# Kernel tuning notes

Measured on AMD Instinct MI355X. Metric: run time of the kernel, lower is better.

The kernel has to match this reference:

```python
import jax, jax.numpy as jnp
import numpy as np

PAD_MAG = 1e12
EPS = 1e-7  # matches prev_step.add_(1e-07) in the torch code


def setup_inputs() -> dict:
    key = jax.random.key(0)
    k1, k2, k3, k4 = jax.random.split(key, 4)
    B, txt_T, mel_T, n_mel = 16, 320, 2000, 80
    mu_logvar = jax.random.normal(k1, (B, txt_T, 2 * n_mel), dtype=jnp.float32)
    melspec = jax.random.normal(k2, (B, n_mel, mel_T), dtype=jnp.float32)
    text_lengths = jax.random.randint(k3, (B,), txt_T // 2, txt_T + 1).astype(jnp.int32)
    mel_lengths = jax.random.randint(k4, (B,), mel_T // 2, mel_T + 1).astype(jnp.int32)
    return {"mu_logvar": mu_logvar, "melspec": melspec,
            "text_lengths": text_lengths, "mel_lengths": mel_lengths}


def _log_prob_matrix(mu_logvar, melspec):
    # exponential[b,j,t] = -0.5 * mean_c( (x[b,t,c]-mu[b,j,c])^2 / exp(logvar) + logvar )
    # avoiding the [B,txt_T,mel_T,n_mel] broadcast the torch code materializes.
    n_mel = melspec.shape[1]
    mu = mu_logvar[:, :, :n_mel]          # [B, txt_T, n_mel]
    logvar = mu_logvar[:, :, n_mel:]      # [B, txt_T, n_mel]
    x = jnp.swapaxes(melspec, 1, 2)       # [B, mel_T, n_mel]
    inv_var = jnp.exp(-logvar)
    xx = jnp.einsum('btc,bjc->bjt', x * x, inv_var)
    xm = jnp.einsum('btc,bjc->bjt', x, mu * inv_var)
    mm = jnp.sum(mu * mu * inv_var + logvar, axis=2)  # [B, txt_T]
    return (-0.5 / n_mel) * (xx - 2.0 * xm + mm[:, :, None])  # [B, txt_T, mel_T]


def _forward_dp(log_prob, text_lengths, mel_lengths):
    # monotonic alignment forward algorithm (logsumexp DP over mel frames)
    B, txt_T, mel_T = log_prob.shape
    # carry = log_alpha column of size txt_T+1 (row 0 is the -inf pad row)
    init = jnp.full((B, txt_T + 1), -PAD_MAG, log_prob.dtype)
    init = init.at[:, 1].set(log_prob[:, 0, 0])

    def step(a, lp):  # a: [B, txt_T+1], lp: [B, txt_T]
        prev = jnp.stack([a[:, 1:], a[:, :-1]], axis=-1) + EPS
        tail = jax.nn.logsumexp(prev, axis=-1) + lp      # [B, txt_T]
        a_new = jnp.concatenate(
            [jnp.full((B, 1), -PAD_MAG, a.dtype), tail], axis=1)
        return a_new, tail

    lps = jnp.moveaxis(log_prob[:, :, 1:], 2, 0)         # [mel_T-1, B, txt_T]
    _, tails = jax.lax.scan(step, init, lps)             # [mel_T-1, B, txt_T]
    log_alpha = jnp.concatenate([init[None, :, 1:], tails], axis=0)  # [mel_T, B, txt_T]
    log_alpha = jnp.moveaxis(log_alpha, 0, 2)            # [B, txt_T, mel_T]

    bidx = jnp.arange(B)
    alpha_last = log_alpha[bidx, text_lengths - 1, mel_lengths - 1]
    alpha_last = alpha_last / mel_lengths.astype(log_alpha.dtype)
    return -jnp.mean(alpha_last)


def reference(mu_logvar, melspec, text_lengths, mel_lengths):
    log_prob = _log_prob_matrix(mu_logvar, melspec)
    mdn_loss = _forward_dp(log_prob, text_lengths, mel_lengths)
    return (mdn_loss, log_prob)
```

## Files before the change

### kernel.cpp

```cpp
#include <hip/hip_runtime.h>

#define BATCH 16
#define TXT   320
#define NMELC 80
#define MELT  2000
#define PADM  1.0e12f
#define L2E   1.4426950408889634f
#define LN2   0.6931471805599453f
#define EPSL2 1.4426950e-7f

typedef __attribute__((ext_vector_type(8))) short bf16x8;
typedef __attribute__((ext_vector_type(4))) float f32x4;

__device__ __forceinline__ short f2bf(float x) {
    unsigned u = __float_as_uint(x);
    unsigned r = (u + 0x7FFFu + ((u >> 16) & 1u)) >> 16;
    return (short)r;
}

__global__ __launch_bounds__(256) void lp_kernel(
    const float* __restrict__ mlv,
    const float* __restrict__ ms,
    float* __restrict__ out_lp)
{
    __shared__ short Ash[20][64][8];
    __shared__ short Bsh[20][128][8];
    __shared__ float bias_p[256];
    __shared__ float bias_s[64];

    const int b   = blockIdx.z;
    const int j0  = blockIdx.y * 64;
    const int t0  = blockIdx.x * 128;
    const int tid = threadIdx.x;
    const float s = -0.00625f;

    const float* mlv_b = mlv + (size_t)b * TXT * 160;
    const float* ms_b  = ms  + (size_t)b * NMELC * MELT;

    {
        const int jj = tid >> 2;
        const int q  = tid & 3;
        const float* p = mlv_b + (size_t)(j0 + jj) * 160 + q * 20;
        float part = 0.f;
        #pragma unroll
        for (int c = 0; c < 20; ++c) {
            float mu = p[c];
            float lv = p[c + 80];
            float iv = __expf(-lv);
            part += mu * mu * iv + lv;
        }
        bias_p[tid] = part;
    }
    __syncthreads();
    if (tid < 64) {
        float v = bias_p[tid * 4] + bias_p[tid * 4 + 1] +
                  bias_p[tid * 4 + 2] + bias_p[tid * 4 + 3];
        bias_s[tid] = s * v;
    }

    #pragma unroll
    for (int pass = 0; pass < 20; ++pass) {
        int idx = pass * 256 + tid;
        int j = idx / 80;
        int c = idx - j * 80;
        float mu = mlv_b[(size_t)(j0 + j) * 160 + c];
        float lv = mlv_b[(size_t)(j0 + j) * 160 + 80 + c];
        float iv = __expf(-lv);
        Ash[c >> 3][j][c & 7]        = f2bf(s * iv);
        Ash[10 + (c >> 3)][j][c & 7] = f2bf(-2.f * s * mu * iv);
    }
    #pragma unroll
    for (int pass = 0; pass < 10; ++pass) {
        int c   = pass * 8 + (tid >> 5);
        int t4i = tid & 31;
        int t   = t0 + t4i * 4;
        float xv[4];
        if (t + 3 < MELT) {
            float4 v = *(const float4*)&ms_b[(size_t)c * MELT + t];
            xv[0] = v.x; xv[1] = v.y; xv[2] = v.z; xv[3] = v.w;
        } else {
            #pragma unroll
            for (int i = 0; i < 4; ++i)
                xv[i] = (t + i < MELT) ? ms_b[(size_t)c * MELT + t + i] : 0.f;
        }
        #pragma unroll
        for (int i = 0; i < 4; ++i) {
            Bsh[c >> 3][t4i * 4 + i][c & 7]        = f2bf(xv[i] * xv[i]);
            Bsh[10 + (c >> 3)][t4i * 4 + i][c & 7] = f2bf(xv[i]);
        }
    }
    __syncthreads();

    const int wv = tid >> 6;
    const int l  = tid & 63;
    const int lr = l & 15;
    const int lg = l >> 4;

    f32x4 acc[8];
    #pragma unroll
    for (int f = 0; f < 8; ++f) acc[f] = (f32x4){0.f, 0.f, 0.f, 0.f};

    #pragma unroll
    for (int ks = 0; ks < 5; ++ks) {
        const int kb = ks * 4 + lg;
        bf16x8 a = *(const bf16x8*)&Ash[kb][wv * 16 + lr][0];
        #pragma unroll
        for (int f = 0; f < 8; ++f) {
            bf16x8 bb = *(const bf16x8*)&Bsh[kb][f * 16 + lr][0];
            acc[f] = __builtin_amdgcn_mfma_f32_16x16x32_bf16(a, bb, acc[f],
                                                             0, 0, 0);
        }
    }

    float bs[4];
    #pragma unroll
    for (int r = 0; r < 4; ++r) bs[r] = bias_s[wv * 16 + lg * 4 + r];
    #pragma unroll
    for (int f = 0; f < 8; ++f) {
        int t = t0 + f * 16 + lr;
        if (t < MELT) {
            #pragma unroll
            for (int r = 0; r < 4; ++r) {
                int j = j0 + wv * 16 + lg * 4 + r;
                out_lp[((size_t)b * TXT + j) * MELT + t] = acc[f][r] + bs[r];
            }
        }
    }
}

__device__ __forceinline__ float dpp_shr1(float x) {
    return __int_as_float(__builtin_amdgcn_update_dpp(
        0, __float_as_int(x), 0x138 , 0xF, 0xF, false));
}

__global__ __launch_bounds__(192, 1) void dp_kernel(
    const float* __restrict__ lp,
    const int* __restrict__ tlen,
    const int* __restrict__ mlen,
    float* __restrict__ res,
    float* __restrict__ out0)
{
    __shared__ float bnd[2][2056];
    __shared__ int   prog[2];

    const int b    = blockIdx.x;
    const int tid  = threadIdx.x;
    const int w    = tid >> 6;
    const int l    = tid & 63;
    const int tend = mlen[b] - 1;
    const int tl   = tlen[b];

    if (tid < 2) prog[tid] = 0;

    int j0c = 2 * tid; if (j0c > 318) j0c = 318;
    const float* r0 = lp + (size_t)(b * TXT + j0c) * MELT;
    const float* r1 = r0 + MELT;

    float A1 = (tid == 0) ? lp[(size_t)b * TXT * MELT] * L2E : -PADM;
    float A2 = -PADM;
    float A1F = A1, A2F = A2;

    if (l == 63 && w < 2) bnd[w][0] = -PADM;
    __syncthreads();

    if (w == 2 && tl < 257) return;

    float ptA2 = -PADM, ptB2 = -PADM;
    const bool is0     = (l == 0);
    const bool isPub   = (l == 63) && (w < 2);
    const bool hasRing = (w > 0);
    int seen = 0;

    const int imax = tend + 63;

    float PA[16], PB[16], PC[16];
    #pragma unroll
    for (int q = 0; q < 8; ++q) { PA[2*q] = r0[1 + q - l]; PA[2*q+1] = r1[1 + q - l]; }
    #pragma unroll
    for (int q = 0; q < 8; ++q) { PB[2*q] = r0[9 + q - l]; PB[2*q+1] = r1[9 + q - l]; }
    #pragma unroll
    for (int q = 0; q < 16; ++q) PA[q] = fmaf(PA[q], L2E, EPSL2);

    const float* p0 = r0 + 17 - l;
    const float* p1 = r1 + 17 - l;

#define RING_RD(BQ_, T0_)                                                    \
    {                                                                        \
        float4 q0_ = *(const float4*)&bnd[w - 1][T0_];                       \
        float4 q1_ = *(const float4*)&bnd[w - 1][(T0_) + 4];                 \
        BQ_[0]=q0_.x; BQ_[1]=q0_.y; BQ_[2]=q0_.z; BQ_[3]=q0_.w;              \
        BQ_[4]=q1_.x; BQ_[5]=q1_.y; BQ_[6]=q1_.z; BQ_[7]=q1_.w;              \
    }
#define RING_POLL(NEED_)                                                     \
    if (seen < (NEED_)) {                                                    \
        int tgt_ = (NEED_) + 32;                                             \
        if (tgt_ > tend - 1) tgt_ = tend - 1;                                \
        if (tgt_ < (NEED_)) tgt_ = (NEED_);                                  \
        volatile int* pv_ = &prog[w - 1];                                    \
        int v_ = *pv_;                                                       \
        while (v_ < tgt_) { __builtin_amdgcn_s_sleep(1); v_ = *pv_; }        \
        seen = v_;                                                           \
        __asm__ volatile("" ::: "memory");                                   \
    }

    float bqC[8];
    if (hasRing) {
        RING_POLL(7)
        RING_RD(bqC, 0)
    } else {
        #pragma unroll
        for (int q = 0; q < 8; ++q) bqC[q] = -PADM;
    }

#define STEP2(Pc_, q_, AQ_)                                                  \
    {                                                                        \
        float pt_ = is0 ? bqC[q_] : ptA2;                                    \
        float m1_ = fmaxf(A1, pt_);                                          \
        float d1_ = A1 - pt_;                                                \
        float e1_ = __builtin_amdgcn_exp2f(-fabsf(d1_));                     \
        float g1_ = __builtin_amdgcn_logf(1.0f + e1_);                       \
        float n1_ = m1_ + g1_ + Pc_[2 * q_];                                 \
        float m2_ = fmaxf(A2, A1);                                           \
        float d2_ = A2 - A1;                                                 \
        float e2_ = __builtin_amdgcn_exp2f(-fabsf(d2_));                     \
        float g2_ = __builtin_amdgcn_logf(1.0f + e2_);                       \
        float n2_ = m2_ + g2_ + Pc_[2 * q_ + 1];                             \
        float ns_ = dpp_shr1(n2_);                                           \
        ptA2 = ptB2; ptB2 = ns_;                                             \
        A1 = n1_; A2 = n2_; AQ_ = n2_;                                       \
    }

#define GROUP2_S(Pc_, Pm_, Pl_, I0_)                                         \
{                                                                            \
    float bqN[8];                                                            \
    if (hasRing) {                                                           \
        const int nt0_ = (I0_) + 7;                                          \
        RING_POLL(nt0_ + 7)                                                  \
        RING_RD(bqN, nt0_)                                                   \
    } else {                                                                 \
        _Pragma("unroll") for (int q_=0;q_<8;++q_) bqN[q_] = -PADM;          \
    }                                                                        \
    _Pragma("unroll") for (int q_=0;q_<8;++q_) {                             \
        Pl_[2*q_] = p0[q_]; Pl_[2*q_+1] = p1[q_];                            \
    }                                                                        \
    float aq2[8];                                                            \
    _Pragma("unroll")                                                        \
    for (int q_=0;q_<8;++q_) STEP2(Pc_, q_, aq2[q_])                         \
    if (isPub) {                                                             \
        const int t63_ = (I0_) - 63;                                         \
        if (t63_ >= 1) {                                                     \
            _Pragma("unroll") for (int q_=0;q_<8;++q_)                       \
                bnd[w][t63_ + q_] = aq2[q_];                                 \
        } else {                                                             \
            _Pragma("unroll") for (int q_=0;q_<8;++q_)                       \
                if (t63_ + q_ >= 1) bnd[w][t63_ + q_] = aq2[q_];             \
        }                                                                    \
        __asm__ volatile("" ::: "memory");          \
        int pgv_ = t63_ + 7;                                                 \
        if (pgv_ >= 1) prog[w] = pgv_;                                       \
    }                                                                        \
    p0 += 8; p1 += 8;                                                        \
    _Pragma("unroll") for (int q_=0;q_<16;++q_)                              \
        Pm_[q_] = fmaf(Pm_[q_], L2E, EPSL2);                                 \
    _Pragma("unroll") for (int q_=0;q_<8;++q_) bqC[q_] = bqN[q_];            \
}

#define GROUP2_T(Pc_, Pm_, Pl_, I0_)                                         \
{                                                                            \
    float bqN[8];                                                            \
    if (hasRing) {                                                           \
        const int nt0_ = (I0_) + 7;                                          \
        int need_ = nt0_ + 7; if (need_ > tend - 1) need_ = tend - 1;        \
        RING_POLL(need_)                                                     \
        const int rb_ = nt0_ > 2048 ? 2048 : nt0_;                           \
        RING_RD(bqN, rb_)                                                    \
    } else {                                                                 \
        _Pragma("unroll") for (int q_=0;q_<8;++q_) bqN[q_] = -PADM;          \
    }                                                                        \
    _Pragma("unroll") for (int q_=0;q_<8;++q_) {                             \
        int t_ = (I0_) + 16 + q_ - l;                                        \
        t_ = t_ < 0 ? 0 : (t_ > tend ? tend : t_);                           \
        Pl_[2*q_] = r0[t_]; Pl_[2*q_+1] = r1[t_];                            \
    }                                                                        \
    float aq2[8];                                                            \
    const int vt_ = (I0_) - l;                                               \
    _Pragma("unroll")                                                        \
    for (int q_=0;q_<8;++q_) {                                               \
        STEP2(Pc_, q_, aq2[q_])                                              \
        bool c_ = (vt_ + q_ == tend);                                        \
        A1F = c_ ? A1 : A1F;                                                 \
        A2F = c_ ? A2 : A2F;                                                 \
    }                                                                        \
    if (isPub) {                                                             \
        const int t63_ = (I0_) - 63;                                         \
        _Pragma("unroll") for (int q_=0;q_<8;++q_) {                         \
            int tq_ = t63_ + q_;                                             \
            if (tq_ >= 1 && tq_ <= tend) bnd[w][tq_] = aq2[q_];              \
        }                                                                    \
        __asm__ volatile("" ::: "memory");                                   \
        int pgv_ = t63_ + 7; if (pgv_ > tend) pgv_ = tend;                   \
        if (pgv_ >= 1) prog[w] = pgv_;                                       \
    }                                                                        \
    _Pragma("unroll") for (int q_=0;q_<16;++q_)                              \
        Pm_[q_] = fmaf(Pm_[q_], L2E, EPSL2);                                 \
    _Pragma("unroll") for (int q_=0;q_<8;++q_) bqC[q_] = bqN[q_];            \
}

    int i0 = 1;
    const int sEnd = tend - 23;
    int ph = 0;
    while (i0 <= sEnd) {
        GROUP2_S(PA, PB, PC, i0); i0 += 8;
        if (i0 > sEnd) { ph = 1; break; }
        GROUP2_S(PB, PC, PA, i0); i0 += 8;
        if (i0 > sEnd) { ph = 2; break; }
        GROUP2_S(PC, PA, PB, i0); i0 += 8;
    }
    if (ph == 1) {
        #pragma unroll
        for (int q = 0; q < 16; ++q) {
            float tmp = PA[q]; PA[q] = PB[q]; PB[q] = PC[q]; PC[q] = tmp;
        }
    } else if (ph == 2) {
        #pragma unroll
        for (int q = 0; q < 16; ++q) {
            float tmp = PA[q]; PA[q] = PC[q]; PC[q] = PB[q]; PB[q] = tmp;
        }
    }
    while (i0 <= imax) {
        GROUP2_T(PA, PB, PC, i0); i0 += 8;
        if (i0 > imax) break;
        GROUP2_T(PB, PC, PA, i0); i0 += 8;
        if (i0 > imax) break;
        GROUP2_T(PC, PA, PB, i0); i0 += 8;
    }

#undef GROUP2_S
#undef GROUP2_T
#undef STEP2
#undef RING_RD
#undef RING_POLL

    if (tid == ((tl - 1) >> 1)) {
        float Af = ((tl - 1) & 1) ? A2F : A1F;
        float v = Af * LN2 / (float)(tend + 1);
        if (res) res[b] = v;
        else     atomicAdd(out0, -v / (float)BATCH);
    }
}

__global__ void zero1_kernel(float* out0) { out0[0] = 0.f; }

__global__ void fin_kernel(const float* __restrict__ res, float* __restrict__ out0)
{
    int l = threadIdx.x;
    float v = (l < BATCH) ? res[l] : 0.f;
    #pragma unroll
    for (int off = 32; off; off >>= 1) v += __shfl_down(v, off);
    if (l == 0) out0[0] = -(v / (float)BATCH);
}

extern "C" void kernel_launch(void* const* d_in, const int* in_sizes, int n_in,
                              void* d_out, int out_size, void* d_ws, size_t ws_size,
                              hipStream_t stream)
{
    const float* mlv = (const float*)d_in[0];
    const float* ms  = (const float*)d_in[1];
    const int*   tl  = (const int*)d_in[2];
    const int*   ml  = (const int*)d_in[3];
    float* out    = (float*)d_out;
    float* out_lp = out + 1;

    bool res_ok = ws_size >= 64;
    float* res = res_ok ? (float*)d_ws : nullptr;

    dim3 gA(16, 5, 16);
    lp_kernel<<<gA, 256, 0, stream>>>(mlv, ms, out_lp);

    if (!res_ok) zero1_kernel<<<1, 1, 0, stream>>>(out);
    dp_kernel<<<BATCH, 192, 0, stream>>>(out_lp, tl, ml, res, out);
    if (res_ok) fin_kernel<<<1, 64, 0, stream>>>(res, out);
}
```

Baseline: 208.5 us.

## Fuse log-prob GEMM and DP into one kernel with per-chunk readiness flags

```diff
diff --git a/kernel.cpp b/kernel.cpp
--- a/kernel.cpp
+++ b/kernel.cpp
@@ -17,20 +17,20 @@
     unsigned r = (u + 0x7FFFu + ((u >> 16) & 1u)) >> 16;
     return (short)r;
 }
-
-__global__ __launch_bounds__(256) void lp_kernel(
-    const float* __restrict__ mlv,
-    const float* __restrict__ ms,
-    float* __restrict__ out_lp)
-{
-    __shared__ short Ash[20][64][8];
-    __shared__ short Bsh[20][128][8];
-    __shared__ float bias_p[256];
-    __shared__ float bias_s[64];
-
-    const int b   = blockIdx.z;
-    const int j0  = blockIdx.y * 64;
-    const int t0  = blockIdx.x * 128;
+__device__ __forceinline__ float dpp_shr1(float x) {
+    return __int_as_float(__builtin_amdgcn_update_dpp(
+        0, __float_as_int(x), 0x138 , 0xF, 0xF, false));
+}
+
+__device__ __forceinline__ void lp_block(
+    const float* __restrict__ mlv, const float* __restrict__ ms,
+    float* __restrict__ out_lp, int b, int j0, int t0, char* SM)
+{
+    short (*Ash)[64][8]  = (short(*)[64][8])SM;
+    short (*Bsh)[128][8] = (short(*)[128][8])(SM + 20480);
+    float* bias_p = (float*)(SM + 61440);
+    float* bias_s = (float*)(SM + 62464);
+
     const int tid = threadIdx.x;
     const float s = -0.00625f;
 
@@ -128,22 +128,14 @@
     }
 }
 
-__device__ __forceinline__ float dpp_shr1(float x) {
-    return __int_as_float(__builtin_amdgcn_update_dpp(
-        0, __float_as_int(x), 0x138 , 0xF, 0xF, false));
-}
-
-__global__ __launch_bounds__(192, 1) void dp_kernel(
-    const float* __restrict__ lp,
-    const int* __restrict__ tlen,
-    const int* __restrict__ mlen,
-    float* __restrict__ res,
-    float* __restrict__ out0)
-{
-    __shared__ float bnd[2][2056];
-    __shared__ int   prog[2];
-
-    const int b    = blockIdx.x;
+__device__ __forceinline__ void dp_block(
+    const float* __restrict__ lp, const int* __restrict__ tlen,
+    const int* __restrict__ mlen, float* __restrict__ res,
+    float* __restrict__ out0, int b, char* SM, int* flags)
+{
+    float (*bnd)[2056] = (float(*)[2056])SM;
+    int* prog = (int*)(SM + 16448);
+
     const int tid  = threadIdx.x;
     const int w    = tid >> 6;
     const int l    = tid & 63;
@@ -151,6 +143,17 @@
     const int tl   = tlen[b];
 
     if (tid < 2) prog[tid] = 0;
+    if (l == 63 && w < 2) bnd[w][0] = -PADM;
+    __syncthreads();
+    if (tid >= 192) return;
+
+#define CHUNK_WAIT(C_)                                                       \
+    while (__hip_atomic_load(&flags[(b << 3) + (C_)], __ATOMIC_ACQUIRE,      \
+                             __HIP_MEMORY_SCOPE_AGENT) < 10)                 \
+        __builtin_amdgcn_s_sleep(8);
+
+    int lastC = 0;
+    if (flags) { CHUNK_WAIT(0) }
 
     int j0c = 2 * tid; if (j0c > 318) j0c = 318;
     const float* r0 = lp + (size_t)(b * TXT + j0c) * MELT;
@@ -159,9 +162,6 @@
     float A1 = (tid == 0) ? lp[(size_t)b * TXT * MELT] * L2E : -PADM;
     float A2 = -PADM;
     float A1F = A1, A2F = A2;
-
-    if (l == 63 && w < 2) bnd[w][0] = -PADM;
-    __syncthreads();
 
     if (w == 2 && tl < 257) return;
 
@@ -201,6 +201,11 @@
         while (v_ < tgt_) { __builtin_amdgcn_s_sleep(1); v_ = *pv_; }        \
         seen = v_;                                                           \
         __asm__ volatile("" ::: "memory");                                   \
+    }
+#define CHUNK_STEP(I0_)                                                      \
+    if (flags) {                                                             \
+        int cN_ = ((I0_) + 31) >> 8; if (cN_ > 7) cN_ = 7;                   \
+        while (lastC < cN_) { ++lastC; CHUNK_WAIT(lastC) }                   \
     }
 
     float bqC[8];
@@ -232,6 +237,7 @@
 
 #define GROUP2_S(Pc_, Pm_, Pl_, I0_)                                         \
 {                                                                            \
+    CHUNK_STEP(I0_)                                                          \
     float bqN[8];                                                            \
     if (hasRing) {                                                           \
         const int nt0_ = (I0_) + 7;                                          \
@@ -267,6 +273,7 @@
 
 #define GROUP2_T(Pc_, Pm_, Pl_, I0_)                                         \
 {                                                                            \
+    CHUNK_STEP(I0_)                                                          \
     float bqN[8];                                                            \
     if (hasRing) {                                                           \
         const int nt0_ = (I0_) + 7;                                          \
@@ -340,6 +347,8 @@
 #undef STEP2
 #undef RING_RD
 #undef RING_POLL
+#undef CHUNK_STEP
+#undef CHUNK_WAIT
 
     if (tid == ((tl - 1) >> 1)) {
         float Af = ((tl - 1) & 1) ? A2F : A1F;
@@ -349,7 +358,54 @@
     }
 }
 
-__global__ void zero1_kernel(float* out0) { out0[0] = 0.f; }
+__global__ __launch_bounds__(256) void fused_kernel(
+    const float* __restrict__ mlv, const float* __restrict__ ms,
+    float* __restrict__ out_lp,
+    const int* __restrict__ tlen, const int* __restrict__ mlen,
+    float* __restrict__ res, int* __restrict__ flags)
+{
+    __shared__ __align__(16) char SM[62720];
+    const int blk = blockIdx.x;
+    if (blk < BATCH) {
+        dp_block(out_lp, tlen, mlen, res, nullptr, blk, SM, flags);
+        return;
+    }
+    const int r   = blk - BATCH;
+    const int c8  = r / 160;
+    const int rem = r % 160;
+    const int b   = rem / 10;
+    const int sub = rem % 10;
+    const int jt  = sub >> 1;
+    const int th  = sub & 1;
+    lp_block(mlv, ms, out_lp, b, jt * 64, c8 * 256 + th * 128, SM);
+    __syncthreads();
+    if (threadIdx.x == 0)
+        __hip_atomic_fetch_add(&flags[(b << 3) + c8], 1,
+                               __ATOMIC_RELEASE, __HIP_MEMORY_SCOPE_AGENT);
+}
+
+__global__ __launch_bounds__(256) void lp_kernel(
+    const float* __restrict__ mlv, const float* __restrict__ ms,
+    float* __restrict__ out_lp)
+{
+    __shared__ __align__(16) char SM[62720];
+    lp_block(mlv, ms, out_lp, blockIdx.z, blockIdx.y * 64, blockIdx.x * 128, SM);
+}
+
+__global__ __launch_bounds__(256) void dp_kernel_fb(
+    const float* __restrict__ lp, const int* __restrict__ tlen,
+    const int* __restrict__ mlen, float* __restrict__ res,
+    float* __restrict__ out0)
+{
+    __shared__ __align__(16) char SM[62720];
+    dp_block(lp, tlen, mlen, res, out0, blockIdx.x, SM, nullptr);
+}
+
+__global__ void init_kernel(int* flags, float* out0, int zero_out)
+{
+    if (threadIdx.x < 128) flags[threadIdx.x] = 0;
+    if (threadIdx.x == 0 && zero_out) out0[0] = 0.f;
+}
 
 __global__ void fin_kernel(const float* __restrict__ res, float* __restrict__ out0)
 {
@@ -371,13 +427,21 @@
     float* out    = (float*)d_out;
     float* out_lp = out + 1;
 
-    bool res_ok = ws_size >= 64;
-    float* res = res_ok ? (float*)d_ws : nullptr;
-
-    dim3 gA(16, 5, 16);
-    lp_kernel<<<gA, 256, 0, stream>>>(mlv, ms, out_lp);
-
-    if (!res_ok) zero1_kernel<<<1, 1, 0, stream>>>(out);
-    dp_kernel<<<BATCH, 192, 0, stream>>>(out_lp, tl, ml, res, out);
-    if (res_ok) fin_kernel<<<1, 64, 0, stream>>>(res, out);
-}
+    bool res_ok   = ws_size >= 64;
+    bool fused_ok = ws_size >= 64 + 512;
+    float* res  = res_ok ? (float*)d_ws : nullptr;
+    int*  flags = fused_ok ? (int*)((char*)d_ws + 64) : nullptr;
+
+    if (fused_ok) {
+        init_kernel<<<1, 128, 0, stream>>>(flags, out, 0);
+        fused_kernel<<<BATCH + 1280, 256, 0, stream>>>(
+            mlv, ms, out_lp, tl, ml, res, flags);
+        fin_kernel<<<1, 64, 0, stream>>>(res, out);
+    } else {
+        dim3 gA(16, 5, 16);
+        lp_kernel<<<gA, 256, 0, stream>>>(mlv, ms, out_lp);
+        if (!res_ok) init_kernel<<<1, 1, 0, stream>>>((int*)d_ws, out, 1);
+        dp_kernel_fb<<<BATCH, 256, 0, stream>>>(out_lp, tl, ml, res, out);
+        if (res_ok) fin_kernel<<<1, 64, 0, stream>>>(res, out);
+    }
+}
```

New measurement: 236.4 us. +13.4%, slower.
